# Kernel optimization log

Measured on AMD Instinct MI355X. Metric: run time of the kernel, lower is better.

## Reference

```python
import jax, jax.numpy as jnp
import numpy as np

N_NODES = 40000
N_EDGES = 640000
HIDDEN = 128
HEADS = 8
HEAD_DIM = HIDDEN // HEADS
SCALING = HEAD_DIM ** (-0.5)
EPS = 1e-5


def _linear_params(key, din, dout):
    kw, kb = jax.random.split(key)
    s = 1.0 / np.sqrt(din)
    W = jax.random.uniform(kw, (din, dout), jnp.float32, -s, s)
    b = jax.random.uniform(kb, (dout,), jnp.float32, -s, s)
    return W, b


def setup_inputs() -> dict:
    key = jax.random.key(0)
    ks = jax.random.split(key, 10)
    h = jax.random.normal(ks[0], (N_NODES, HIDDEN), jnp.float32)
    row = jax.random.randint(ks[1], (N_EDGES,), 0, N_NODES)
    col = jax.random.randint(ks[2], (N_EDGES,), 0, N_NODES)
    Wq, bq = _linear_params(ks[3], HIDDEN, HIDDEN)
    Wk, bk = _linear_params(ks[4], HIDDEN, HIDDEN)
    Wv, bv = _linear_params(ks[5], HIDDEN, HIDDEN)
    Wo, bo = _linear_params(ks[6], HIDDEN, HIDDEN)
    W1, bf1 = _linear_params(ks[7], HIDDEN, 2 * HIDDEN)
    W2, bf2 = _linear_params(ks[8], 2 * HIDDEN, HIDDEN)
    g1 = jnp.ones((HIDDEN,), jnp.float32)
    b1 = jnp.zeros((HIDDEN,), jnp.float32)
    g2 = jnp.ones((HIDDEN,), jnp.float32)
    b2 = jnp.zeros((HIDDEN,), jnp.float32)
    return {"h": h, "row": row, "col": col,
            "Wq": Wq, "bq": bq, "Wk": Wk, "bk": bk, "Wv": Wv, "bv": bv,
            "Wo": Wo, "bo": bo, "W1": W1, "bf1": bf1, "W2": W2, "bf2": bf2,
            "g1": g1, "b1": b1, "g2": g2, "b2": b2}


def _batchnorm(x, g, b):
    # training-mode BatchNorm1d over node axis (biased variance)
    mu = jnp.mean(x, axis=0)
    var = jnp.mean((x - mu) ** 2, axis=0)
    return (x - mu) * jax.lax.rsqrt(var + EPS) * g + b


def reference(h, row, col, Wq, bq, Wk, bk, Wv, bv, Wo, bo, W1, bf1, W2, bf2, g1, b1, g2, b2):
    N = h.shape[0]
    # QKV projections, reshaped to (N, head_dim, heads) matching the torch code
    q = ((h @ Wq + bq).reshape(N, HEAD_DIM, HEADS)) * SCALING
    k = (h @ Wk + bk).reshape(N, HEAD_DIM, HEADS)
    v = (h @ Wv + bv).reshape(N, HEAD_DIM, HEADS)
    # bsddmm: per-edge, per-head scores  s[e,h] = sum_d q[row,d,h]*k[col,d,h]
    s = jnp.einsum("edh,edh->eh", q[row], k[col])  # [E, H]
    # sparse softmax over each destination row segment
    m = jax.ops.segment_max(s, row, num_segments=N)  # [N, H]
    e = jnp.exp(s - m[row])
    z = jax.ops.segment_sum(e, row, num_segments=N)  # [N, H]
    attn = e / z[row]  # [E, H]
    # bspmm: out[i,d,h] = sum_{e: row[e]=i} attn[e,h] * v[col[e],d,h]
    out = jax.ops.segment_sum(attn[:, None, :] * v[col], row, num_segments=N)  # [N, Dh, H]
    out = out.reshape(N, HIDDEN) @ Wo + bo
    # residual + BN + GELU
    x = _batchnorm(out + h, g1, b1)
    x = jax.nn.gelu(x, approximate=False)
    # FFN with residual
    y = jax.nn.gelu(x @ W1 + bf1, approximate=False) @ W2 + bf2
    return _batchnorm(x + y, g2, b2)
```

## Files before the change

kernel.cpp:

```cpp
#include <hip/hip_runtime.h>

#define N_NODES 40000
#define N_EDGES 640000
#define HID 128
#define NHEAD 8

typedef __attribute__((ext_vector_type(8))) short short8;
typedef __attribute__((ext_vector_type(4))) short short4v;
typedef __attribute__((ext_vector_type(4))) float f32x4;

static constexpr size_t OFF_QB   = 0;
static constexpr size_t OFF_KV8  = 10240000;
static constexpr size_t OFF_AOB  = 20480000;
static constexpr size_t OFF_XB   = 30720000;
static constexpr size_t OFF_TB   = 40960000;
static constexpr size_t OFF_HB   = 61440000;
static constexpr size_t OFF_WQKV = 71680000;
static constexpr size_t OFF_WTO  = 71778304;
static constexpr size_t OFF_WT1  = 71811072;
static constexpr size_t OFF_WT2  = 71876608;
static constexpr size_t OFF_BQKV = 71942144;
static constexpr size_t OFF_DEG  = 72000000;
static constexpr size_t OFF_OFFS = 72160000;
static constexpr size_t OFF_CUR  = 72320000;
static constexpr size_t OFF_COLW = 72480000;
static constexpr size_t OFF_BSUM = 75040000;
static constexpr size_t OFF_ST   = 75041024;

__device__ inline unsigned short f2b(float f) {
    unsigned x = __float_as_uint(f);
    unsigned r = x + 0x7fffu + ((x >> 16) & 1u);
    return (unsigned short)(r >> 16);
}
__device__ inline float b2f(unsigned short u) {
    return __uint_as_float(((unsigned)u) << 16);
}
__device__ inline unsigned char f2fp8(float f) {
    return (unsigned char)(__builtin_amdgcn_cvt_pk_fp8_f32(f, f, 0, false) & 0xff);
}

__global__ void h2b_kernel(const float* __restrict__ h, unsigned short* __restrict__ hb)
{
    const int i = (blockIdx.x * 256 + threadIdx.x) * 8;
    float4 f0 = *(const float4*)(h + i);
    float4 f1 = *(const float4*)(h + i + 4);
    short8 w;
    w[0] = (short)f2b(f0.x); w[1] = (short)f2b(f0.y);
    w[2] = (short)f2b(f0.z); w[3] = (short)f2b(f0.w);
    w[4] = (short)f2b(f1.x); w[5] = (short)f2b(f1.y);
    w[6] = (short)f2b(f1.z); w[7] = (short)f2b(f1.w);
    *(short8*)(hb + i) = w;
}

__global__ void wt_kernel(const float* __restrict__ Wq, const float* __restrict__ Wk,
                          const float* __restrict__ Wv, const float* __restrict__ Wo,
                          const float* __restrict__ W1, const float* __restrict__ W2,
                          const float* __restrict__ bq, const float* __restrict__ bk,
                          const float* __restrict__ bv,
                          unsigned short* __restrict__ WTqkv, unsigned short* __restrict__ WTo,
                          unsigned short* __restrict__ WT1, unsigned short* __restrict__ WT2,
                          float* __restrict__ bqkv)
{
    int i = blockIdx.x * 256 + threadIdx.x;
    if (i < 16384) {
        int k = i >> 7, n = i & 127;
        WTqkv[n * 128 + k] = f2b(0.25f * Wq[i]);
    } else if (i < 32768) {
        int j = i - 16384; int k = j >> 7, n = j & 127;
        WTqkv[(128 + n) * 128 + k] = f2b(Wk[j]);
    } else if (i < 49152) {
        int j = i - 32768; int k = j >> 7, n = j & 127;
        WTqkv[(256 + n) * 128 + k] = f2b(Wv[j]);
    } else if (i < 65536) {
        int j = i - 49152; int k = j >> 7, n = j & 127;
        WTo[n * 128 + k] = f2b(Wo[j]);
    } else if (i < 98304) {
        int j = i - 65536; int k = j >> 8, n = j & 255;
        WT1[n * 128 + k] = f2b(W1[j]);
    } else {
        int j = i - 98304; int k = j >> 7, n = j & 127;
        WT2[n * 256 + k] = f2b(W2[j]);
    }
    if (blockIdx.x == 0 && threadIdx.x < 384) {
        int c = threadIdx.x;
        float v = (c < 128) ? 0.25f * bq[c] : (c < 256) ? bk[c - 128] : bv[c - 256];
        bqkv[c] = v;
    }
}

template<typename TC, typename TR, int K, int NTOT, bool ACT, bool STATS, bool QKVMODE>
__global__ __launch_bounds__(256) void mm_kernel(
    const unsigned short* __restrict__ A, const unsigned short* __restrict__ WT,
    const float* __restrict__ bias, const TR* __restrict__ res,
    TC* __restrict__ C, unsigned char* __restrict__ kv8, float* __restrict__ st)
{
    __shared__ unsigned short As[64][136];
    __shared__ unsigned short Bs[128][136];
    const int t = threadIdx.x;
    const int lane = t & 63, wave = t >> 6;
    const int row0 = blockIdx.x * 64;
    const int colOff = blockIdx.y * 128;

    f32x4 acc[4][2];
#pragma unroll
    for (int i = 0; i < 4; ++i)
#pragma unroll
        for (int j = 0; j < 2; ++j) acc[i][j] = (f32x4){0.f, 0.f, 0.f, 0.f};

    for (int k0 = 0; k0 < K; k0 += 128) {
        {
            const int r = t >> 2, kc = (t & 3) * 32;
            const unsigned short* ap = A + (size_t)(row0 + r) * K + k0 + kc;
#pragma unroll
            for (int i = 0; i < 4; ++i)
                *(short8*)&As[r][kc + 8 * i] = *(const short8*)(ap + 8 * i);
        }
        {
            const int n = t >> 1, kc = (t & 1) * 64;
            const unsigned short* wp = WT + (size_t)(colOff + n) * K + k0 + kc;
#pragma unroll
            for (int i = 0; i < 8; ++i)
                *(short8*)&Bs[n][kc + 8 * i] = *(const short8*)(wp + 8 * i);
        }
        __syncthreads();

#pragma unroll
        for (int ks = 0; ks < 4; ++ks) {
            const int kf = ks * 32 + (lane >> 4) * 8;
            short8 af[4], bf_[2];
#pragma unroll
            for (int mi = 0; mi < 4; ++mi)
                af[mi] = *(short8*)&As[mi * 16 + (lane & 15)][kf];
#pragma unroll
            for (int ni = 0; ni < 2; ++ni)
                bf_[ni] = *(short8*)&Bs[wave * 32 + ni * 16 + (lane & 15)][kf];
#pragma unroll
            for (int mi = 0; mi < 4; ++mi)
#pragma unroll
                for (int ni = 0; ni < 2; ++ni)
                    acc[mi][ni] = __builtin_amdgcn_mfma_f32_16x16x32_bf16(
                        af[mi], bf_[ni], acc[mi][ni], 0, 0, 0);
        }
        __syncthreads();
    }

    float csum[2] = {0.f, 0.f}, csq[2] = {0.f, 0.f};
#pragma unroll
    for (int mi = 0; mi < 4; ++mi) {
#pragma unroll
        for (int ni = 0; ni < 2; ++ni) {
            const int lc = wave * 32 + ni * 16 + (lane & 15);
            const int c = colOff + lc;
            const float bv_ = bias[c];
#pragma unroll
            for (int reg = 0; reg < 4; ++reg) {
                const int r = row0 + mi * 16 + (lane >> 4) * 4 + reg;
                float val = acc[mi][ni][reg] + bv_;
                if constexpr (!__is_same(TR, void)) {
                    if constexpr (sizeof(TR) == 4)
                        val += ((const float*)res)[(size_t)r * 128 + c];
                    else
                        val += b2f(((const unsigned short*)res)[(size_t)r * 128 + c]);
                }
                if constexpr (ACT)
                    val = 0.5f * val * (1.0f + erff(val * 0.70710678118654752f));
                if constexpr (STATS) {
                    csum[ni] += val;
                    csq[ni]  += val * val;
                }
                if constexpr (QKVMODE) {
                    if (colOff == 0) {
                        ((unsigned short*)C)[(size_t)r * 128 + lc] = f2b(val);
                    } else {
                        const int idx = (lc >> 1) * 4 + (lc & 1) + ((colOff == 256) ? 2 : 0);
                        kv8[(size_t)r * 256 + idx] = f2fp8(val);
                    }
                } else {
                    if constexpr (sizeof(TC) == 4)
                        ((float*)C)[(size_t)r * NTOT + c] = val;
                    else
                        ((unsigned short*)C)[(size_t)r * NTOT + c] = f2b(val);
                }
            }
        }
    }

    if constexpr (STATS) {
#pragma unroll
        for (int ni = 0; ni < 2; ++ni) {
            float s = csum[ni], qq = csq[ni];
            s  += __shfl_xor(s, 16, 64);  s  += __shfl_xor(s, 32, 64);
            qq += __shfl_xor(qq, 16, 64); qq += __shfl_xor(qq, 32, 64);
            if (lane < 16) {
                const int c = wave * 32 + ni * 16 + lane;
                atomicAdd(st + c, s);
                atomicAdd(st + 128 + c, qq);
            }
        }
    }
}

__global__ void count_kernel(const int* __restrict__ row, int* __restrict__ deg)
{
    int e = blockIdx.x * 256 + threadIdx.x;
    if (e < N_EDGES) atomicAdd(deg + row[e], 1);
}

__global__ __launch_bounds__(256) void bsum_kernel(const int* __restrict__ deg,
                                                   int* __restrict__ bsum)
{
    __shared__ int ws[4];
    int idx = blockIdx.x * 256 + threadIdx.x;
    int v = (idx < N_NODES) ? deg[idx] : 0;
#pragma unroll
    for (int ofs = 1; ofs < 64; ofs <<= 1) v += __shfl_xor(v, ofs, 64);
    if ((threadIdx.x & 63) == 0) ws[threadIdx.x >> 6] = v;
    __syncthreads();
    if (threadIdx.x == 0) bsum[blockIdx.x] = ws[0] + ws[1] + ws[2] + ws[3];
}

__global__ __launch_bounds__(256) void scan2_kernel(const int* __restrict__ deg,
                                                    const int* __restrict__ bsum,
                                                    int* __restrict__ offs,
                                                    int* __restrict__ cur)
{
    __shared__ int wsum[4];
    __shared__ int base_s;
    const int t = threadIdx.x, lane = t & 63, w = t >> 6;

    int p = 0;
    for (int i = t; i < blockIdx.x; i += 256) p += bsum[i];
#pragma unroll
    for (int ofs = 1; ofs < 64; ofs <<= 1) p += __shfl_xor(p, ofs, 64);
    if (lane == 0) wsum[w] = p;
    __syncthreads();
    if (t == 0) base_s = wsum[0] + wsum[1] + wsum[2] + wsum[3];
    __syncthreads();

    int idx = blockIdx.x * 256 + t;
    int v = (idx < N_NODES) ? deg[idx] : 0;
    int x = v;
#pragma unroll
    for (int d = 1; d < 64; d <<= 1) {
        int y = __shfl_up(x, d, 64);
        if (lane >= d) x += y;
    }
    __syncthreads();
    if (lane == 63) wsum[w] = x;
    __syncthreads();
    int pre = base_s;
    for (int i = 0; i < w; ++i) pre += wsum[i];
    int excl = pre + x - v;
    if (idx < N_NODES) { offs[idx] = excl; cur[idx] = excl; }
}

__global__ void scatter_kernel(const int* __restrict__ row, const int* __restrict__ col,
                               int* __restrict__ cursor, int* __restrict__ colw)
{
    int e = blockIdx.x * 256 + threadIdx.x;
    if (e < N_EDGES) {
        int pos = atomicAdd(cursor + row[e], 1);
        colw[pos] = col[e] * 64;
    }
}

__global__ __launch_bounds__(256) void attn_kernel(
    const unsigned short* __restrict__ qb, const unsigned* __restrict__ kv8,
    const int* __restrict__ colw, const int* __restrict__ offs,
    const int* __restrict__ deg, unsigned short* __restrict__ aob)
{
    const int node = blockIdx.x * 4 + (threadIdx.x >> 6);
    const int lane = threadIdx.x & 63;
    const int c0 = 2 * lane;
    const int start = offs[node];
    const int d = deg[node];

    unsigned qu = *(const unsigned*)(qb + (size_t)node * 128 + c0);
    float q0 = __uint_as_float(qu << 16);
    float q1 = __uint_as_float(qu & 0xffff0000u);
    float z0 = 0.f, z1 = 0.f, o0 = 0.f, o1 = 0.f;

#define ATTN_EDGE_W(W)                                                  \
    {                                                                   \
        float p0 = q0 * __builtin_amdgcn_cvt_f32_fp8((int)(W), 0);      \
        float p1 = q1 * __builtin_amdgcn_cvt_f32_fp8((int)(W), 1);      \
        _Pragma("unroll")                                               \
        for (int ofs = 4; ofs < 64; ofs <<= 1) {                        \
            p0 += __shfl_xor(p0, ofs, 64);                              \
            p1 += __shfl_xor(p1, ofs, 64);                              \
        }                                                               \
        float e0 = __expf(p0), e1 = __expf(p1);                         \
        z0 += e0; z1 += e1;                                             \
        o0 = fmaf(e0, __builtin_amdgcn_cvt_f32_fp8((int)(W), 2), o0);   \
        o1 = fmaf(e1, __builtin_amdgcn_cvt_f32_fp8((int)(W), 3), o1);   \
    }

    for (int base = 0; base < d; base += 64) {
        const int nrem = min(64, d - base);
        int cls = 0;
        if (lane < nrem) cls = colw[start + base + lane];
        int j = 0;
        for (; j + 8 <= nrem; j += 8) {
            unsigned w[8];
#pragma unroll
            for (int u = 0; u < 8; ++u) {
                int cs = __shfl(cls, j + u, 64);
                w[u] = kv8[cs + lane];
            }
#pragma unroll
            for (int u = 0; u < 8; ++u) ATTN_EDGE_W(w[u]);
        }
        for (; j < nrem; ++j) {
            int cs = __shfl(cls, j, 64);
            unsigned w = kv8[cs + lane];
            ATTN_EDGE_W(w);
        }
    }
    float r0 = (d > 0) ? o0 / z0 : 0.f;
    float r1 = (d > 0) ? o1 / z1 : 0.f;
    *(unsigned*)(aob + (size_t)node * HID + c0) =
        (unsigned)f2b(r0) | ((unsigned)f2b(r1) << 16);
}

template<typename TO, bool ACT>
__global__ void bn_kernel(const float* __restrict__ x, const float* __restrict__ st,
                          const float* __restrict__ g, const float* __restrict__ b,
                          TO* __restrict__ out)
{
    const int i = (blockIdx.x * 256 + threadIdx.x) * 4;
    const int c = i & (HID - 1);
    float4 xv = *(const float4*)(x + i);
    float v[4] = {xv.x, xv.y, xv.z, xv.w};
#pragma unroll
    for (int u = 0; u < 4; ++u) {
        const int cc = c + u;
        float mu  = st[cc] * (1.0f / N_NODES);
        float var = st[HID + cc] * (1.0f / N_NODES) - mu * mu;
        float val = (v[u] - mu) * rsqrtf(var + 1e-5f) * g[cc] + b[cc];
        if constexpr (ACT) val = 0.5f * val * (1.0f + erff(val * 0.70710678118654752f));
        v[u] = val;
    }
    if constexpr (sizeof(TO) == 4) {
        *(float4*)((float*)out + i) = (float4){v[0], v[1], v[2], v[3]};
    } else {
        short4v w;
        w[0] = (short)f2b(v[0]); w[1] = (short)f2b(v[1]);
        w[2] = (short)f2b(v[2]); w[3] = (short)f2b(v[3]);
        *(short4v*)((unsigned short*)out + i) = w;
    }
}

extern "C" void kernel_launch(void* const* d_in, const int* in_sizes, int n_in,
                              void* d_out, int out_size, void* d_ws, size_t ws_size,
                              hipStream_t stream)
{
    const float* h   = (const float*)d_in[0];
    const int*   row = (const int*)d_in[1];
    const int*   col = (const int*)d_in[2];
    const float* Wq  = (const float*)d_in[3];
    const float* bq  = (const float*)d_in[4];
    const float* Wk  = (const float*)d_in[5];
    const float* bk  = (const float*)d_in[6];
    const float* Wv  = (const float*)d_in[7];
    const float* bv  = (const float*)d_in[8];
    const float* Wo  = (const float*)d_in[9];
    const float* bo  = (const float*)d_in[10];
    const float* W1  = (const float*)d_in[11];
    const float* bf1 = (const float*)d_in[12];
    const float* W2  = (const float*)d_in[13];
    const float* bf2 = (const float*)d_in[14];
    const float* g1  = (const float*)d_in[15];
    const float* b1  = (const float*)d_in[16];
    const float* g2  = (const float*)d_in[17];
    const float* b2  = (const float*)d_in[18];

    float* out = (float*)d_out;
    char*  ws  = (char*)d_ws;

    unsigned short* qb   = (unsigned short*)(ws + OFF_QB);
    unsigned char*  kv8  = (unsigned char*)(ws + OFF_KV8);
    unsigned short* aob  = (unsigned short*)(ws + OFF_AOB);
    unsigned short* xb   = (unsigned short*)(ws + OFF_XB);
    unsigned short* tb   = (unsigned short*)(ws + OFF_TB);
    unsigned short* hb   = (unsigned short*)(ws + OFF_HB);
    unsigned short* WTqkv= (unsigned short*)(ws + OFF_WQKV);
    unsigned short* WTo  = (unsigned short*)(ws + OFF_WTO);
    unsigned short* WT1  = (unsigned short*)(ws + OFF_WT1);
    unsigned short* WT2  = (unsigned short*)(ws + OFF_WT2);
    float* bqkv = (float*)(ws + OFF_BQKV);
    int*   deg  = (int*)(ws + OFF_DEG);
    int*   offs = (int*)(ws + OFF_OFFS);
    int*   cur  = (int*)(ws + OFF_CUR);
    int*   colw = (int*)(ws + OFF_COLW);
    int*   bsum = (int*)(ws + OFF_BSUM);
    float* st1  = (float*)(ws + OFF_ST);
    float* st2  = st1 + 256;

    hipMemsetAsync(ws + OFF_DEG, 0, (size_t)N_NODES * 4, stream);
    hipMemsetAsync(ws + OFF_ST,  0, 2048, stream);

    dim3 blk(256);
    const int nScanBlocks = (N_NODES + 255) / 256;

    wt_kernel<<<dim3(512), blk, 0, stream>>>(Wq, Wk, Wv, Wo, W1, W2, bq, bk, bv,
                                             WTqkv, WTo, WT1, WT2, bqkv);
    h2b_kernel<<<dim3(2500), blk, 0, stream>>>(h, hb);

    mm_kernel<unsigned short, void, 128, 384, false, false, true>
        <<<dim3(625, 3), blk, 0, stream>>>(hb, WTqkv, bqkv, nullptr, qb, kv8, nullptr);

    count_kernel<<<dim3(N_EDGES / 256), blk, 0, stream>>>(row, deg);
    bsum_kernel<<<dim3(nScanBlocks), blk, 0, stream>>>(deg, bsum);
    scan2_kernel<<<dim3(nScanBlocks), blk, 0, stream>>>(deg, bsum, offs, cur);
    scatter_kernel<<<dim3(N_EDGES / 256), blk, 0, stream>>>(row, col, cur, colw);

    attn_kernel<<<dim3(N_NODES / 4), blk, 0, stream>>>(qb, (const unsigned*)kv8,
                                                       colw, offs, deg, aob);

    mm_kernel<float, unsigned short, 128, 128, false, true, false>
        <<<dim3(625, 1), blk, 0, stream>>>(aob, WTo, bo, hb, out, nullptr, st1);

    bn_kernel<unsigned short, true>
        <<<dim3(N_NODES * HID / 1024), blk, 0, stream>>>(out, st1, g1, b1, xb);

    mm_kernel<unsigned short, void, 128, 256, true, false, false>
        <<<dim3(625, 2), blk, 0, stream>>>(xb, WT1, bf1, nullptr, tb, nullptr, nullptr);

    mm_kernel<float, unsigned short, 256, 128, false, true, false>
        <<<dim3(625, 1), blk, 0, stream>>>(tb, WT2, bf2, xb, out, nullptr, st2);

    bn_kernel<float, false>
        <<<dim3(N_NODES * HID / 1024), blk, 0, stream>>>(out, st2, g2, b2, out);
}
```

Baseline: 258.3 us.

## Use head-major QKV layout and per-lane head-slice attention with staged stores

Permutes the Q/K/V weight columns and Wo rows so each head's 16 features are contiguous, letting the attention kernel give each lane one head and one of eight edges. Each lane then loads 16-byte K and V slices, computes the full per-head dot product locally, and the cross-lane shuffle reduction runs only once per node instead of per edge. The QKV GEMM epilogue stages results in shared memory and writes them out as coalesced 16-byte rows instead of scattered scalar stores. It costs more registers per lane (16 accumulators plus q), and a partial final group of edges leaves some lanes idle.

```diff
diff --git a/kernel.cpp b/kernel.cpp
--- a/kernel.cpp
+++ b/kernel.cpp
@@ -38,6 +38,7 @@
 __device__ inline unsigned char f2fp8(float f) {
     return (unsigned char)(__builtin_amdgcn_cvt_pk_fp8_f32(f, f, 0, false) & 0xff);
 }
+__device__ inline int hmpos(int n) { return (n & 7) * 16 + (n >> 3); }
 
 __global__ void h2b_kernel(const float* __restrict__ h, unsigned short* __restrict__ hb)
 {
@@ -64,16 +65,16 @@
     int i = blockIdx.x * 256 + threadIdx.x;
     if (i < 16384) {
         int k = i >> 7, n = i & 127;
-        WTqkv[n * 128 + k] = f2b(0.25f * Wq[i]);
+        WTqkv[hmpos(n) * 128 + k] = f2b(0.25f * Wq[i]);
     } else if (i < 32768) {
         int j = i - 16384; int k = j >> 7, n = j & 127;
-        WTqkv[(128 + n) * 128 + k] = f2b(Wk[j]);
+        WTqkv[(128 + hmpos(n)) * 128 + k] = f2b(Wk[j]);
     } else if (i < 49152) {
         int j = i - 32768; int k = j >> 7, n = j & 127;
-        WTqkv[(256 + n) * 128 + k] = f2b(Wv[j]);
+        WTqkv[(256 + hmpos(n)) * 128 + k] = f2b(Wv[j]);
     } else if (i < 65536) {
         int j = i - 49152; int k = j >> 7, n = j & 127;
-        WTo[n * 128 + k] = f2b(Wo[j]);
+        WTo[n * 128 + hmpos(k)] = f2b(Wo[j]);
     } else if (i < 98304) {
         int j = i - 65536; int k = j >> 8, n = j & 255;
         WT1[n * 128 + k] = f2b(W1[j]);
@@ -83,8 +84,9 @@
     }
     if (blockIdx.x == 0 && threadIdx.x < 384) {
         int c = threadIdx.x;
-        float v = (c < 128) ? 0.25f * bq[c] : (c < 256) ? bk[c - 128] : bv[c - 256];
-        bqkv[c] = v;
+        int seg = c >> 7, n = c & 127;
+        float v = (seg == 0) ? 0.25f * bq[n] : (seg == 1) ? bk[n] : bv[n];
+        bqkv[seg * 128 + hmpos(n)] = v;
     }
 }
 
@@ -144,6 +146,9 @@
         __syncthreads();
     }
 
+    unsigned short* LQ  = (unsigned short*)&As[0][0];
+    unsigned char*  LKV = (unsigned char*)&As[0][0];
+
     float csum[2] = {0.f, 0.f}, csq[2] = {0.f, 0.f};
 #pragma unroll
     for (int mi = 0; mi < 4; ++mi) {
@@ -154,7 +159,8 @@
             const float bv_ = bias[c];
 #pragma unroll
             for (int reg = 0; reg < 4; ++reg) {
-                const int r = row0 + mi * 16 + (lane >> 4) * 4 + reg;
+                const int rl = mi * 16 + (lane >> 4) * 4 + reg;
+                const int r = row0 + rl;
                 float val = acc[mi][ni][reg] + bv_;
                 if constexpr (!__is_same(TR, void)) {
                     if constexpr (sizeof(TR) == 4)
@@ -169,12 +175,8 @@
                     csq[ni]  += val * val;
                 }
                 if constexpr (QKVMODE) {
-                    if (colOff == 0) {
-                        ((unsigned short*)C)[(size_t)r * 128 + lc] = f2b(val);
-                    } else {
-                        const int idx = (lc >> 1) * 4 + (lc & 1) + ((colOff == 256) ? 2 : 0);
-                        kv8[(size_t)r * 256 + idx] = f2fp8(val);
-                    }
+                    if (colOff == 0) LQ[rl * 128 + lc] = f2b(val);
+                    else             LKV[rl * 128 + lc] = f2fp8(val);
                 } else {
                     if constexpr (sizeof(TC) == 4)
                         ((float*)C)[(size_t)r * NTOT + c] = val;
@@ -182,6 +184,21 @@
                         ((unsigned short*)C)[(size_t)r * NTOT + c] = f2b(val);
                 }
             }
+        }
+    }
+
+    if constexpr (QKVMODE) {
+        __syncthreads();
+        const int rrow = t >> 2, ch = t & 3;
+        if (colOff == 0) {
+            uint4* dst = (uint4*)((unsigned short*)C + (size_t)(row0 + rrow) * 128 + ch * 32);
+            const uint4* src = (const uint4*)(LQ + rrow * 128 + ch * 32);
+            dst[0] = src[0]; dst[1] = src[1]; dst[2] = src[2]; dst[3] = src[3];
+        } else {
+            const int segbase = (colOff == 128) ? 0 : 128;
+            uint4* dst = (uint4*)(kv8 + (size_t)(row0 + rrow) * 256 + segbase + ch * 32);
+            const uint4* src = (const uint4*)(LKV + rrow * 128 + ch * 32);
+            dst[0] = src[0]; dst[1] = src[1];
         }
     }
 
@@ -260,66 +277,87 @@
     int e = blockIdx.x * 256 + threadIdx.x;
     if (e < N_EDGES) {
         int pos = atomicAdd(cursor + row[e], 1);
-        colw[pos] = col[e] * 64;
+        colw[pos] = col[e] * 256;
     }
 }
 
 __global__ __launch_bounds__(256) void attn_kernel(
-    const unsigned short* __restrict__ qb, const unsigned* __restrict__ kv8,
+    const unsigned short* __restrict__ qh, const unsigned char* __restrict__ kv8,
     const int* __restrict__ colw, const int* __restrict__ offs,
     const int* __restrict__ deg, unsigned short* __restrict__ aob)
 {
     const int node = blockIdx.x * 4 + (threadIdx.x >> 6);
     const int lane = threadIdx.x & 63;
-    const int c0 = 2 * lane;
+    const int h = lane & 7;
+    const int es = lane >> 3;
     const int start = offs[node];
     const int d = deg[node];
 
-    unsigned qu = *(const unsigned*)(qb + (size_t)node * 128 + c0);
-    float q0 = __uint_as_float(qu << 16);
-    float q1 = __uint_as_float(qu & 0xffff0000u);
-    float z0 = 0.f, z1 = 0.f, o0 = 0.f, o1 = 0.f;
-
-#define ATTN_EDGE_W(W)                                                  \
-    {                                                                   \
-        float p0 = q0 * __builtin_amdgcn_cvt_f32_fp8((int)(W), 0);      \
-        float p1 = q1 * __builtin_amdgcn_cvt_f32_fp8((int)(W), 1);      \
-        _Pragma("unroll")                                               \
-        for (int ofs = 4; ofs < 64; ofs <<= 1) {                        \
-            p0 += __shfl_xor(p0, ofs, 64);                              \
-            p1 += __shfl_xor(p1, ofs, 64);                              \
-        }                                                               \
-        float e0 = __expf(p0), e1 = __expf(p1);                         \
-        z0 += e0; z1 += e1;                                             \
-        o0 = fmaf(e0, __builtin_amdgcn_cvt_f32_fp8((int)(W), 2), o0);   \
-        o1 = fmaf(e1, __builtin_amdgcn_cvt_f32_fp8((int)(W), 3), o1);   \
-    }
+    float qv[16];
+    {
+        const uint4* qp = (const uint4*)(qh + (size_t)node * 128 + h * 16);
+        uint4 a = qp[0], b = qp[1];
+        unsigned uu[8] = {a.x, a.y, a.z, a.w, b.x, b.y, b.z, b.w};
+#pragma unroll
+        for (int i = 0; i < 8; ++i) {
+            qv[2 * i]     = __uint_as_float(uu[i] << 16);
+            qv[2 * i + 1] = __uint_as_float(uu[i] & 0xffff0000u);
+        }
+    }
+    float z = 0.f;
+    float o[16];
+#pragma unroll
+    for (int i = 0; i < 16; ++i) o[i] = 0.f;
 
     for (int base = 0; base < d; base += 64) {
         const int nrem = min(64, d - base);
-        int cls = 0;
-        if (lane < nrem) cls = colw[start + base + lane];
-        int j = 0;
-        for (; j + 8 <= nrem; j += 8) {
-            unsigned w[8];
-#pragma unroll
-            for (int u = 0; u < 8; ++u) {
-                int cs = __shfl(cls, j + u, 64);
-                w[u] = kv8[cs + lane];
+        int cl = 0;
+        if (lane < nrem) cl = colw[start + base + lane];
+        for (int j = 0; j < nrem; j += 8) {
+            const int idx = j + es;
+            const int cs = __shfl(cl, idx, 64);
+            const bool valid = idx < nrem;
+            uint4 kw = *(const uint4*)(kv8 + cs + h * 16);
+            uint4 vw = *(const uint4*)(kv8 + cs + 128 + h * 16);
+            unsigned kk[4] = {kw.x, kw.y, kw.z, kw.w};
+            unsigned vv[4] = {vw.x, vw.y, vw.z, vw.w};
+            float p0 = 0.f, p1 = 0.f, p2 = 0.f, p3 = 0.f;
+#pragma unroll
+            for (int w = 0; w < 4; ++w) {
+                p0 = fmaf(qv[4 * w + 0], __builtin_amdgcn_cvt_f32_fp8((int)kk[w], 0), p0);
+                p1 = fmaf(qv[4 * w + 1], __builtin_amdgcn_cvt_f32_fp8((int)kk[w], 1), p1);
+                p2 = fmaf(qv[4 * w + 2], __builtin_amdgcn_cvt_f32_fp8((int)kk[w], 2), p2);
+                p3 = fmaf(qv[4 * w + 3], __builtin_amdgcn_cvt_f32_fp8((int)kk[w], 3), p3);
             }
-#pragma unroll
-            for (int u = 0; u < 8; ++u) ATTN_EDGE_W(w[u]);
-        }
-        for (; j < nrem; ++j) {
-            int cs = __shfl(cls, j, 64);
-            unsigned w = kv8[cs + lane];
-            ATTN_EDGE_W(w);
-        }
-    }
-    float r0 = (d > 0) ? o0 / z0 : 0.f;
-    float r1 = (d > 0) ? o1 / z1 : 0.f;
-    *(unsigned*)(aob + (size_t)node * HID + c0) =
-        (unsigned)f2b(r0) | ((unsigned)f2b(r1) << 16);
+            const float p = (p0 + p1) + (p2 + p3);
+            const float e = valid ? __expf(p) : 0.f;
+            z += e;
+#pragma unroll
+            for (int w = 0; w < 4; ++w) {
+                o[4 * w + 0] = fmaf(e, __builtin_amdgcn_cvt_f32_fp8((int)vv[w], 0), o[4 * w + 0]);
+                o[4 * w + 1] = fmaf(e, __builtin_amdgcn_cvt_f32_fp8((int)vv[w], 1), o[4 * w + 1]);
+                o[4 * w + 2] = fmaf(e, __builtin_amdgcn_cvt_f32_fp8((int)vv[w], 2), o[4 * w + 2]);
+                o[4 * w + 3] = fmaf(e, __builtin_amdgcn_cvt_f32_fp8((int)vv[w], 3), o[4 * w + 3]);
+            }
+        }
+    }
+
+#pragma unroll
+    for (int m = 8; m < 64; m <<= 1) {
+        z += __shfl_xor(z, m, 64);
+#pragma unroll
+        for (int i = 0; i < 16; ++i) o[i] += __shfl_xor(o[i], m, 64);
+    }
+    if (es == 0) {
+        const float rz = (d > 0) ? 1.f / z : 0.f;
+        short8 w0, w1;
+#pragma unroll
+        for (int i = 0; i < 8; ++i) w0[i] = (short)f2b(o[i] * rz);
+#pragma unroll
+        for (int i = 0; i < 8; ++i) w1[i] = (short)f2b(o[8 + i] * rz);
+        *(short8*)(aob + (size_t)node * 128 + h * 16)     = w0;
+        *(short8*)(aob + (size_t)node * 128 + h * 16 + 8) = w1;
+    }
 }
 
 template<typename TO, bool ACT>
@@ -377,7 +415,7 @@
     float* out = (float*)d_out;
     char*  ws  = (char*)d_ws;
 
-    unsigned short* qb   = (unsigned short*)(ws + OFF_QB);
+    unsigned short* qh   = (unsigned short*)(ws + OFF_QB);
     unsigned char*  kv8  = (unsigned char*)(ws + OFF_KV8);
     unsigned short* aob  = (unsigned short*)(ws + OFF_AOB);
     unsigned short* xb   = (unsigned short*)(ws + OFF_XB);
@@ -407,15 +445,14 @@
     h2b_kernel<<<dim3(2500), blk, 0, stream>>>(h, hb);
 
     mm_kernel<unsigned short, void, 128, 384, false, false, true>
-        <<<dim3(625, 3), blk, 0, stream>>>(hb, WTqkv, bqkv, nullptr, qb, kv8, nullptr);
+        <<<dim3(625, 3), blk, 0, stream>>>(hb, WTqkv, bqkv, nullptr, qh, kv8, nullptr);
 
     count_kernel<<<dim3(N_EDGES / 256), blk, 0, stream>>>(row, deg);
     bsum_kernel<<<dim3(nScanBlocks), blk, 0, stream>>>(deg, bsum);
     scan2_kernel<<<dim3(nScanBlocks), blk, 0, stream>>>(deg, bsum, offs, cur);
     scatter_kernel<<<dim3(N_EDGES / 256), blk, 0, stream>>>(row, col, cur, colw);
 
-    attn_kernel<<<dim3(N_NODES / 4), blk, 0, stream>>>(qb, (const unsigned*)kv8,
-                                                       colw, offs, deg, aob);
+    attn_kernel<<<dim3(N_NODES / 4), blk, 0, stream>>>(qh, kv8, colw, offs, deg, aob);
 
     mm_kernel<float, unsigned short, 128, 128, false, true, false>
         <<<dim3(625, 1), blk, 0, stream>>>(aob, WTo, bo, hb, out, nullptr, st1);
```

After: 227.1 us. 1.14x faster.
